# Optimization experiments

Hardware: AMD Instinct MI355X
Metric: run time of the kernel (lower is better)

The kernel has to match this reference:

```python
import jax, jax.numpy as jnp
import numpy as np

L_S = 4  # segment length (== factor in __init__)


def dtw_dist(x, y):
    """Exact 1-D DTW distance with |a-b| cost (the quantity fastdtw approximates).

    Row recurrence d[i,j] = C[i,j] + min(d[i-1,j], d[i-1,j-1], d[i,j-1]) is
    solved per row in closed form: with a[j]=min(prev[j],prev[j-1]),
    b[j]=C[i,j]+a[j], S=cumsum(C[i]), we have d[i,:] = S + cummin(b - S).
    """
    C = jnp.abs(x[:, None] - y[None, :])  # [n, m] cost matrix
    big = jnp.asarray(jnp.finfo(C.dtype).max, C.dtype)
    row0 = jnp.cumsum(C[0])  # first DP row: cumulative cost

    def step(prev, c):
        shifted = jnp.concatenate([jnp.full((1,), big, prev.dtype), prev[:-1]])
        a = jnp.minimum(prev, shifted)          # min(d[i-1,j], d[i-1,j-1])
        S = jnp.cumsum(c)
        d = S + jax.lax.cummin(a + c - S)       # min-plus prefix scan
        return d, None

    last, _ = jax.lax.scan(step, row0, C[1:])
    return last[-1]


def setup_inputs() -> dict:
    key = jax.random.key(0)
    kq, kk, kv = jax.random.split(key, 3)
    B, L, H, D = 1, 32, 8, 32
    return {
        "queries": jax.random.normal(kq, (B, L, H, D), dtype=jnp.float32),
        "keys": jax.random.normal(kk, (B, L, H, D), dtype=jnp.float32),
        "values": jax.random.normal(kv, (B, L, H, D), dtype=jnp.float32),
        "attn_mask": jnp.zeros((1,), dtype=bool),  # unused, as in original
    }


def reference(queries, keys, values, attn_mask):
    B, Lq, H, D = queries.shape
    Lk = keys.shape[1]
    Ls = L_S
    scale = 1.0 / np.sqrt(Ls).astype(np.float32)
    Nq, Nk = Lq // Ls, Lk // Ls  # L divisible by Ls -> no addition_Q path

    seg_q = queries.reshape(B, Nq, Ls, H, D)
    seg_k = keys.reshape(B, Nk, Ls, H, D)
    seg_v = values.reshape(B, Nk, Ls, H, D)

    # Original flattens each segment over (B, Ls, H, D) before fastdtw, so the
    # distance is identical for every (b, h): a single [Nq, Nk] matrix.
    flat_q = jnp.moveaxis(seg_q, 1, 0).reshape(Nq, -1)  # [Nq, B*Ls*H*D]
    flat_k = jnp.moveaxis(seg_k, 1, 0).reshape(Nk, -1)  # [Nk, B*Ls*H*D]

    dists = jax.vmap(lambda xq: jax.vmap(lambda xk: dtw_dist(xq, xk))(flat_k))(flat_q)  # [Nq, Nk]

    A = jax.nn.softmax(scale * dists, axis=-1)  # [Nq, Nk], broadcast over (B, H)

    # Softmax-weighted sum of value segments (intended semantics of the
    # expanded matmul): V[b,i,t,h,d] = sum_j A[i,j] * seg_v[b,j,t,h,d]
    V = jnp.einsum('ij,bjthd->bithd', A, seg_v).reshape(B, Nq * Ls, H, D)
    return V
```

## Files before the change

kernel.cpp:

```cpp
#include <hip/hip_runtime.h>
#include <float.h>

#define NSEG 8
#define SEGLEN 1024
#define BIGV 1e30f
#define PADV 1e18f

#define NW 4
#define CH 64
#define NCH 17
#define XLEN 1152
#define BSTRIDE 1160

#define DPPF(OLD, SRC, CTRL, RM, BM, BC)                                      \
    __int_as_float(__builtin_amdgcn_update_dpp(                               \
        __float_as_int(OLD), __float_as_int(SRC), CTRL, RM, BM, BC))
#define WSHIFT1(OLD, SRC) DPPF(OLD, SRC, 0x138, 0xF, 0xF, false)

__device__ __forceinline__ float readlaneF(float v, int l) {
    return __int_as_float(__builtin_amdgcn_readlane(__float_as_int(v), l));
}

__global__ __launch_bounds__(256) void dtw_sk4_kernel(const float* __restrict__ q,
                                                      const float* __restrict__ kk,
                                                      float* __restrict__ dists) {
    __shared__ float xl[XLEN];
    __shared__ float bnd[NW + 1][BSTRIDE];
    __shared__ float dump[128];
    __shared__ int flagsA[NW + 1];
    const int tid = threadIdx.x;
    const int lane = tid & 63;
    const int wv = tid >> 6;
    const int pair = blockIdx.x;
    const float* __restrict__ x = q + (pair >> 3) * SEGLEN;
    const float* __restrict__ y = kk + (pair & 7) * SEGLEN;

    for (int t = tid; t < XLEN; t += 256) xl[t] = (t < SEGLEN) ? x[t] : PADV;
    for (int t = tid; t < (NW + 1) * BSTRIDE; t += 256)
        (&bnd[0][0])[t] = (t == 63) ? 0.f : BIGV;
    if (tid < NW + 1) flagsA[tid] = (tid == 0) ? 0x7FFFFFFF : 0;

    const float4 y4 = *(const float4*)(y + wv * 256 + lane * 4);
    const float yv0 = y4.x, yv1 = y4.y, yv2 = y4.z, yv3 = y4.w;

    __syncthreads();

    const float* __restrict__ br = &bnd[wv][0];

    {
        const int need0 = (NCH < 2) ? NCH : 2;
        while (__hip_atomic_load(&flagsA[wv], __ATOMIC_ACQUIRE,
                                 __HIP_MEMORY_SCOPE_WORKGROUP) < need0)
            __builtin_amdgcn_s_sleep(1);
    }
    float P0 = BIGV, P1 = BIGV, P2 = BIGV, P3 = BIGV, xreg = PADV;
    float lf = br[64];
    float dgl = br[63];

#define STEP(s, xp, bp) {                                                     \
    xreg = WSHIFT1(xp, xreg);                                                 \
    const float c0n = fabsf(xreg - yv0) + fminf(fminf(P0, lf), dgl);          \
    const float c1n = fabsf(xreg - yv1) + fminf(fminf(P1, c0n), P0);          \
    const float c2n = fabsf(xreg - yv2) + fminf(fminf(P2, c1n), P1);          \
    const float c3n = fabsf(xreg - yv3) + fminf(fminf(P3, c2n), P2);          \
    const float n1 = WSHIFT1(bp, c3n);                                        \
    dgl = lf; lf = n1; P0 = c0n; P1 = c1n; P2 = c2n; P3 = c3n;                \
    va[(s)] = c3n;                                                            \
}
#define STEP8(s) {                                                            \
    const float xp0 = readlaneF(xv, (s)+0), xp1 = readlaneF(xv, (s)+1);       \
    const float xp2 = readlaneF(xv, (s)+2), xp3 = readlaneF(xv, (s)+3);       \
    const float xp4 = readlaneF(xv, (s)+4), xp5 = readlaneF(xv, (s)+5);       \
    const float xp6 = readlaneF(xv, (s)+6), xp7 = readlaneF(xv, (s)+7);       \
    const float bp0 = readlaneF(bvv, (s)+0), bp1 = readlaneF(bvv, (s)+1);     \
    const float bp2 = readlaneF(bvv, (s)+2), bp3 = readlaneF(bvv, (s)+3);     \
    const float bp4 = readlaneF(bvv, (s)+4), bp5 = readlaneF(bvv, (s)+5);     \
    const float bp6 = readlaneF(bvv, (s)+6), bp7 = readlaneF(bvv, (s)+7);     \
    STEP((s)+0, xp0, bp0) STEP((s)+1, xp1, bp1)                               \
    STEP((s)+2, xp2, bp2) STEP((s)+3, xp3, bp3)                               \
    STEP((s)+4, xp4, bp4) STEP((s)+5, xp5, bp5)                               \
    STEP((s)+6, xp6, bp6) STEP((s)+7, xp7, bp7)                               \
}

#pragma unroll 1
    for (int tc = 0; tc < NCH; ++tc) {
        const int need = (tc + 2 < NCH) ? (tc + 2) : NCH;
        while (__hip_atomic_load(&flagsA[wv], __ATOMIC_ACQUIRE,
                                 __HIP_MEMORY_SCOPE_WORKGROUP) < need)
            __builtin_amdgcn_s_sleep(1);

        const float xv = xl[CH * tc + lane];
        const float bvv = br[CH * tc + 65 + lane];
        float* va = (lane == 63) ? &bnd[wv + 1][CH * tc + 1] : &dump[lane];

        STEP8(0) STEP8(8) STEP8(16) STEP8(24) STEP8(32) STEP8(40) STEP8(48) STEP8(56)

        __hip_atomic_store(&flagsA[wv + 1], tc + 1, __ATOMIC_RELEASE,
                           __HIP_MEMORY_SCOPE_WORKGROUP);
    }
#undef STEP
#undef STEP8

    if (wv == NW - 1 && lane == 0) dists[pair] = bnd[NW][1087];
}

__global__ __launch_bounds__(256) void softmax_out_kernel(const float* __restrict__ v,
                                                          const float* __restrict__ dists,
                                                          float* __restrict__ out) {
    const int o = blockIdx.x * blockDim.x + threadIdx.x;
    if (o >= NSEG * SEGLEN) return;
    const int i = o >> 10;
    const int p = o & 1023;

    float l[NSEG];
    float mx = -FLT_MAX;
#pragma unroll
    for (int j = 0; j < NSEG; ++j) {
        l[j] = 0.5f * dists[i * NSEG + j];
        mx = fmaxf(mx, l[j]);
    }
    float s = 0.f;
#pragma unroll
    for (int j = 0; j < NSEG; ++j) {
        l[j] = expf(l[j] - mx);
        s += l[j];
    }
    const float inv = 1.f / s;
    float acc = 0.f;
#pragma unroll
    for (int j = 0; j < NSEG; ++j) acc += (l[j] * inv) * v[j * SEGLEN + p];
    out[o] = acc;
}

extern "C" void kernel_launch(void* const* d_in, const int* in_sizes, int n_in,
                              void* d_out, int out_size, void* d_ws, size_t ws_size,
                              hipStream_t stream) {
    const float* q = (const float*)d_in[0];
    const float* k = (const float*)d_in[1];
    const float* v = (const float*)d_in[2];
    float* out = (float*)d_out;
    float* dists = (float*)d_ws;

    dtw_sk4_kernel<<<dim3(NSEG * NSEG), dim3(256), 0, stream>>>(q, k, dists);
    softmax_out_kernel<<<dim3((NSEG * SEGLEN + 255) / 256), dim3(256), 0, stream>>>(v, dists, out);
}
```

Measured before the change: 63.83 us.

## Fuse softmax-weighted output into DTW kernel via last-block counter; shorten DP chain

Removes the second kernel launch by having the last DTW block to finish (detected with an atomic counter) compute the softmax weights and the weighted sum over value segments. The per-step recurrence is also rewritten as a min-plus prefix scan over the four columns a lane holds, with prefix sums of the costs. This shortens the serial dependency chain inside each step. The trade-off is that the output stage now runs on a single block, and an extra memset is added to reset the counter.

```diff
diff --git a/kernel.cpp b/kernel.cpp
--- a/kernel.cpp
+++ b/kernel.cpp
@@ -23,11 +23,16 @@
 
 __global__ __launch_bounds__(256) void dtw_sk4_kernel(const float* __restrict__ q,
                                                       const float* __restrict__ kk,
-                                                      float* __restrict__ dists) {
+                                                      const float* __restrict__ vv,
+                                                      float* __restrict__ out,
+                                                      float* __restrict__ dists,
+                                                      int* __restrict__ cnt) {
     __shared__ float xl[XLEN];
     __shared__ float bnd[NW + 1][BSTRIDE];
     __shared__ float dump[128];
     __shared__ int flagsA[NW + 1];
+    __shared__ int lastFlag;
+    __shared__ float wgt[NSEG][NSEG];
     const int tid = threadIdx.x;
     const int lane = tid & 63;
     const int wv = tid >> 6;
@@ -39,6 +44,7 @@
     for (int t = tid; t < (NW + 1) * BSTRIDE; t += 256)
         (&bnd[0][0])[t] = (t == 63) ? 0.f : BIGV;
     if (tid < NW + 1) flagsA[tid] = (tid == 0) ? 0x7FFFFFFF : 0;
+    if (tid == 0) lastFlag = 0;
 
     const float4 y4 = *(const float4*)(y + wv * 256 + lane * 4);
     const float yv0 = y4.x, yv1 = y4.y, yv2 = y4.z, yv3 = y4.w;
@@ -59,13 +65,22 @@
 
 #define STEP(s, xp, bp) {                                                     \
     xreg = WSHIFT1(xp, xreg);                                                 \
-    const float c0n = fabsf(xreg - yv0) + fminf(fminf(P0, lf), dgl);          \
-    const float c1n = fabsf(xreg - yv1) + fminf(fminf(P1, c0n), P0);          \
-    const float c2n = fabsf(xreg - yv2) + fminf(fminf(P2, c1n), P1);          \
-    const float c3n = fabsf(xreg - yv3) + fminf(fminf(P3, c2n), P2);          \
-    const float n1 = WSHIFT1(bp, c3n);                                        \
-    dgl = lf; lf = n1; P0 = c0n; P1 = c1n; P2 = c2n; P3 = c3n;                \
-    va[(s)] = c3n;                                                            \
+    const float ls0 = fabsf(xreg - yv0);                                      \
+    const float ls1 = ls0 + fabsf(xreg - yv1);                                \
+    const float ls2 = ls1 + fabsf(xreg - yv2);                                \
+    const float ls3 = ls2 + fabsf(xreg - yv3);                                \
+    const float a0 = fminf(P0, dgl);                                          \
+    const float a1 = fminf(P1, P0) - ls0;                                     \
+    const float a2 = fminf(P2, P1) - ls1;                                     \
+    const float a3 = fminf(P3, P2) - ls2;                                     \
+    const float r0 = fminf(a0, lf);                                           \
+    const float r1 = fminf(r0, a1);                                           \
+    const float r2 = fminf(r1, a2);                                           \
+    const float r3 = fminf(r2, a3);                                           \
+    P0 = ls0 + r0; P1 = ls1 + r1; P2 = ls2 + r2; P3 = ls3 + r3;               \
+    const float n1 = WSHIFT1(bp, P3);                                         \
+    dgl = lf; lf = n1;                                                        \
+    va[(s)] = P3;                                                             \
 }
 #define STEP8(s) {                                                            \
     const float xp0 = readlaneF(xv, (s)+0), xp1 = readlaneF(xv, (s)+1);       \
@@ -101,35 +116,39 @@
 #undef STEP
 #undef STEP8
 
-    if (wv == NW - 1 && lane == 0) dists[pair] = bnd[NW][1087];
-}
+    if (wv == NW - 1 && lane == 0) {
+        dists[pair] = bnd[NW][1087];
+        __threadfence();
+        int old = __hip_atomic_fetch_add(cnt, 1, __ATOMIC_ACQ_REL,
+                                         __HIP_MEMORY_SCOPE_AGENT);
+        if (old == NSEG * NSEG - 1) lastFlag = 1;
+    }
+    __syncthreads();
+    if (!lastFlag) return;
 
-__global__ __launch_bounds__(256) void softmax_out_kernel(const float* __restrict__ v,
-                                                          const float* __restrict__ dists,
-                                                          float* __restrict__ out) {
-    const int o = blockIdx.x * blockDim.x + threadIdx.x;
-    if (o >= NSEG * SEGLEN) return;
-    const int i = o >> 10;
-    const int p = o & 1023;
-
-    float l[NSEG];
-    float mx = -FLT_MAX;
+    if (tid < NSEG) {
+        float l[NSEG], mx = -FLT_MAX;
 #pragma unroll
-    for (int j = 0; j < NSEG; ++j) {
-        l[j] = 0.5f * dists[i * NSEG + j];
-        mx = fmaxf(mx, l[j]);
+        for (int j = 0; j < NSEG; ++j) {
+            l[j] = 0.5f * dists[tid * NSEG + j];
+            mx = fmaxf(mx, l[j]);
+        }
+        float s = 0.f;
+#pragma unroll
+        for (int j = 0; j < NSEG; ++j) { l[j] = expf(l[j] - mx); s += l[j]; }
+        const float inv = 1.f / s;
+#pragma unroll
+        for (int j = 0; j < NSEG; ++j) wgt[tid][j] = l[j] * inv;
     }
-    float s = 0.f;
+    __syncthreads();
+    for (int o = tid; o < NSEG * SEGLEN; o += 256) {
+        const int i = o >> 10;
+        const int p = o & 1023;
+        float acc = 0.f;
 #pragma unroll
-    for (int j = 0; j < NSEG; ++j) {
-        l[j] = expf(l[j] - mx);
-        s += l[j];
+        for (int j = 0; j < NSEG; ++j) acc += wgt[i][j] * vv[j * SEGLEN + p];
+        out[o] = acc;
     }
-    const float inv = 1.f / s;
-    float acc = 0.f;
-#pragma unroll
-    for (int j = 0; j < NSEG; ++j) acc += (l[j] * inv) * v[j * SEGLEN + p];
-    out[o] = acc;
 }
 
 extern "C" void kernel_launch(void* const* d_in, const int* in_sizes, int n_in,
@@ -140,7 +159,9 @@
     const float* v = (const float*)d_in[2];
     float* out = (float*)d_out;
     float* dists = (float*)d_ws;
+    int* cnt = (int*)((char*)d_ws + 256);
 
-    dtw_sk4_kernel<<<dim3(NSEG * NSEG), dim3(256), 0, stream>>>(q, k, dists);
-    softmax_out_kernel<<<dim3((NSEG * SEGLEN + 255) / 256), dim3(256), 0, stream>>>(v, dists, out);
+    hipMemsetAsync(cnt, 0, sizeof(int), stream);
+    dtw_sk4_kernel<<<dim3(NSEG * NSEG), dim3(256), 0, stream>>>(q, k, v, out,
+                                                                dists, cnt);
 }
```

New measurement: 97.98 us. 1.54x slower.

## Skew DTW wavefront by two steps per lane to hide DPP latency

Applied to the files above, without the earlier changes.

Changes the anti-diagonal skew between adjacent lanes from one to two steps, buffering shifted x values and left-boundary values through a two-deep register delay so each cross-lane DPP result is consumed a step later. This is meant to take DPP shift latency off the serial min-plus dependency chain. It requires one extra chunk per wave, larger padded shared buffers, a new boundary offset, and a looser inter-wave wait condition, which adds pipeline fill work.

```diff
diff --git a/kernel.cpp b/kernel.cpp
--- a/kernel.cpp
+++ b/kernel.cpp
@@ -8,9 +8,10 @@
 
 #define NW 4
 #define CH 64
-#define NCH 17
-#define XLEN 1152
-#define BSTRIDE 1160
+#define NCH 18
+#define XLEN 1216
+#define BOFF 128
+#define BSTRIDE 1288
 
 #define DPPF(OLD, SRC, CTRL, RM, BM, BC)                                      \
     __int_as_float(__builtin_amdgcn_update_dpp(                               \
@@ -21,9 +22,9 @@
     return __int_as_float(__builtin_amdgcn_readlane(__float_as_int(v), l));
 }
 
-__global__ __launch_bounds__(256) void dtw_sk4_kernel(const float* __restrict__ q,
-                                                      const float* __restrict__ kk,
-                                                      float* __restrict__ dists) {
+__global__ __launch_bounds__(256) void dtw_d2_kernel(const float* __restrict__ q,
+                                                     const float* __restrict__ kk,
+                                                     float* __restrict__ dists) {
     __shared__ float xl[XLEN];
     __shared__ float bnd[NW + 1][BSTRIDE];
     __shared__ float dump[128];
@@ -37,7 +38,7 @@
 
     for (int t = tid; t < XLEN; t += 256) xl[t] = (t < SEGLEN) ? x[t] : PADV;
     for (int t = tid; t < (NW + 1) * BSTRIDE; t += 256)
-        (&bnd[0][0])[t] = (t == 63) ? 0.f : BIGV;
+        (&bnd[0][0])[t] = (t == BOFF - 1) ? 0.f : BIGV;
     if (tid < NW + 1) flagsA[tid] = (tid == 0) ? 0x7FFFFFFF : 0;
 
     const float4 y4 = *(const float4*)(y + wv * 256 + lane * 4);
@@ -53,19 +54,25 @@
                                  __HIP_MEMORY_SCOPE_WORKGROUP) < need0)
             __builtin_amdgcn_s_sleep(1);
     }
-    float P0 = BIGV, P1 = BIGV, P2 = BIGV, P3 = BIGV, xreg = PADV;
-    float lf = br[64];
-    float dgl = br[63];
+    float Q0 = BIGV, Q1 = BIGV, Q2 = BIGV, Q3 = BIGV;
+    const float x0u = xl[0], x1u = xl[1];
+    float xA = (lane == 0) ? x0u : PADV;
+    float xB = (lane == 0) ? x1u : PADV;
+    float lf  = br[BOFF];
+    float lfB = br[BOFF + 1];
+    float dgl = br[BOFF - 1];
 
 #define STEP(s, xp, bp) {                                                     \
-    xreg = WSHIFT1(xp, xreg);                                                 \
-    const float c0n = fabsf(xreg - yv0) + fminf(fminf(P0, lf), dgl);          \
-    const float c1n = fabsf(xreg - yv1) + fminf(fminf(P1, c0n), P0);          \
-    const float c2n = fabsf(xreg - yv2) + fminf(fminf(P2, c1n), P1);          \
-    const float c3n = fabsf(xreg - yv3) + fminf(fminf(P3, c2n), P2);          \
-    const float n1 = WSHIFT1(bp, c3n);                                        \
-    dgl = lf; lf = n1; P0 = c0n; P1 = c1n; P2 = c2n; P3 = c3n;                \
-    va[(s)] = c3n;                                                            \
+    const float c0 = fabsf(xA - yv0) + fminf(fminf(Q0, lf), dgl);             \
+    const float c1 = fabsf(xA - yv1) + fminf(fminf(Q1, c0), Q0);              \
+    const float c2 = fabsf(xA - yv2) + fminf(fminf(Q2, c1), Q1);              \
+    const float c3 = fabsf(xA - yv3) + fminf(fminf(Q3, c2), Q2);              \
+    const float tL = WSHIFT1(bp, c3);                                         \
+    const float tX = WSHIFT1(xp, xA);                                         \
+    va[(s)] = c3;                                                             \
+    dgl = lf; lf = lfB; lfB = tL;                                             \
+    xA = xB; xB = tX;                                                         \
+    Q0 = c0; Q1 = c1; Q2 = c2; Q3 = c3;                                       \
 }
 #define STEP8(s) {                                                            \
     const float xp0 = readlaneF(xv, (s)+0), xp1 = readlaneF(xv, (s)+1);       \
@@ -84,14 +91,14 @@
 
 #pragma unroll 1
     for (int tc = 0; tc < NCH; ++tc) {
-        const int need = (tc + 2 < NCH) ? (tc + 2) : NCH;
+        const int need = (tc + 3 < NCH) ? (tc + 3) : NCH;
         while (__hip_atomic_load(&flagsA[wv], __ATOMIC_ACQUIRE,
                                  __HIP_MEMORY_SCOPE_WORKGROUP) < need)
             __builtin_amdgcn_s_sleep(1);
 
-        const float xv = xl[CH * tc + lane];
-        const float bvv = br[CH * tc + 65 + lane];
-        float* va = (lane == 63) ? &bnd[wv + 1][CH * tc + 1] : &dump[lane];
+        const float xv = xl[64 * tc + 2 + lane];
+        const float bvv = br[64 * tc + BOFF + 2 + lane];
+        float* va = (lane == 63) ? &bnd[wv + 1][64 * tc + 2] : &dump[lane];
 
         STEP8(0) STEP8(8) STEP8(16) STEP8(24) STEP8(32) STEP8(40) STEP8(48) STEP8(56)
 
@@ -101,7 +108,7 @@
 #undef STEP
 #undef STEP8
 
-    if (wv == NW - 1 && lane == 0) dists[pair] = bnd[NW][1087];
+    if (wv == NW - 1 && lane == 0) dists[pair] = bnd[NW][1151];
 }
 
 __global__ __launch_bounds__(256) void softmax_out_kernel(const float* __restrict__ v,
@@ -141,6 +148,6 @@
     float* out = (float*)d_out;
     float* dists = (float*)d_ws;
 
-    dtw_sk4_kernel<<<dim3(NSEG * NSEG), dim3(256), 0, stream>>>(q, k, dists);
+    dtw_d2_kernel<<<dim3(NSEG * NSEG), dim3(256), 0, stream>>>(q, k, dists);
     softmax_out_kernel<<<dim3((NSEG * SEGLEN + 255) / 256), dim3(256), 0, stream>>>(v, dists, out);
 }
```

Measured after the change: 73.07 us. +14.5%, slower.
